# Performance work log

Hardware: AMD Instinct MI355X
Metric: run time of the kernel (lower is better)

## Reference

```python
import jax, jax.numpy as jnp
import numpy as np

B, C, D = 32768, 1000, 512
ALPHA, BETA = 1.0, 1.0
TEMPERATURE = 0.1


def setup_inputs() -> dict:
    key = jax.random.key(0)
    k1, k2, k3, k4 = jax.random.split(key, 4)
    return {
        "features_front": jax.random.normal(k1, (B, D), dtype=jnp.float32),
        "logits": jax.random.normal(k2, (B, C), dtype=jnp.float32),
        "labels": jax.random.randint(k3, (B,), 0, C, dtype=jnp.int64),
        "text_prototype": jax.random.normal(k4, (C, D), dtype=jnp.float32),
    }


def reference(features_front, logits, labels, text_prototype):
    num_class = text_prototype.shape[0]

    # F.cross_entropy (mean reduction)
    logp = jax.nn.log_softmax(logits, axis=-1)
    loss_ce = -jnp.mean(jnp.take_along_axis(logp, labels[:, None], axis=1)[:, 0])

    # F.normalize(prototypes, dim=1)
    norm = jnp.linalg.norm(text_prototype, axis=1, keepdims=True)
    prototypes = text_prototype / jnp.maximum(norm, 1e-12)

    # supervised contrastive term against class prototypes
    feat_dot_prototype = (features_front @ prototypes.T) / TEMPERATURE  # [B, C]
    logits_max = jax.lax.stop_gradient(jnp.max(feat_dot_prototype, axis=1, keepdims=True))
    lg = feat_dot_prototype - logits_max
    log_prob = lg - jnp.log(jnp.sum(jnp.exp(lg), axis=1, keepdims=True))
    mask = (labels[:, None] == jnp.arange(num_class)[None, :]).astype(log_prob.dtype)
    mean_log_prob_pos = jnp.sum(mask * log_prob, axis=1)
    simloss = -jnp.mean(mean_log_prob_pos)

    # prototype repulsion: sum_{i != j} exp(p_i . p_j) == masked exp-sum of Gram matrix
    gram = prototypes @ prototypes.T  # [C, C]
    offdiag = 1.0 - jnp.eye(num_class, dtype=gram.dtype)
    textloss = jnp.log(jnp.sum(jnp.exp(gram) * offdiag)) / num_class

    return ALPHA * simloss + BETA * loss_ce + textloss
```

## Files before the change

kernel.cpp:

```cpp
#include <hip/hip_runtime.h>
#include <math.h>

#define NB 32768
#define NC 1000
#define ND 512
#define LOG2E 1.4426950408889634f
#define LN2 0.6931471805599453f
#define S2 14.426950408889634f
#define OFF2 79.3482272f
#define OFFLN 55.0f
#define NBUCKET 64

typedef __attribute__((ext_vector_type(8))) short short8;
typedef __attribute__((ext_vector_type(16))) float f32x16;

__device__ __forceinline__ float fexp2(float x) {
    float r; asm("v_exp_f32 %0, %1" : "=v"(r) : "v"(x)); return r;
}
__device__ __forceinline__ float flog2(float x) {
    float r; asm("v_log_f32 %0, %1" : "=v"(r) : "v"(x)); return r;
}
__device__ __forceinline__ unsigned short bf16_rne(float f) {
    unsigned int u = __builtin_bit_cast(unsigned int, f);
    u += 0x7FFFu + ((u >> 16) & 1u);
    return (unsigned short)(u >> 16);
}
__device__ __forceinline__ short8 pack8f(float4 a, float4 b) {
    short8 s;
    s[0] = (short)bf16_rne(a.x); s[1] = (short)bf16_rne(a.y);
    s[2] = (short)bf16_rne(a.z); s[3] = (short)bf16_rne(a.w);
    s[4] = (short)bf16_rne(b.x); s[5] = (short)bf16_rne(b.y);
    s[6] = (short)bf16_rne(b.z); s[7] = (short)bf16_rne(b.w);
    return s;
}

__device__ __forceinline__ void stage16k(const short8* __restrict__ src, short8* dst, int t) {
#pragma unroll
    for (int s = 0; s < 4; ++s) {
        const int id = t + 256 * s;
        __builtin_amdgcn_global_load_lds(
            (const __attribute__((address_space(1))) unsigned int*)(src + id),
            (__attribute__((address_space(3))) unsigned int*)(dst + id), 16, 0, 0);
    }
}

__global__ __launch_bounds__(256) void norm_protos(const float* __restrict__ pro,
                                                   unsigned short* __restrict__ pbf) {
    const int row = blockIdx.x, t = threadIdx.x;
    const int grp = row >> 5, l31 = row & 31;
    const int ks = t >> 3, h = (t >> 2) & 1, p = t & 3;
    const int k0 = ks * 16 + 8 * h + 2 * p;
    unsigned int* dst = (unsigned int*)pbf +
        ((size_t)(grp * 32 + ks) * 64 + h * 32 + l31) * 4 + p;
    if (row >= NC) { *dst = 0u; return; }
    const float* rp = pro + (size_t)row * ND;
    const float x0 = rp[k0], x1 = rp[k0 + 1];
    float ss = x0 * x0 + x1 * x1;
#pragma unroll
    for (int o = 1; o < 64; o <<= 1) ss += __shfl_xor(ss, o, 64);
    __shared__ float part[4];
    if ((t & 63) == 0) part[t >> 6] = ss;
    __syncthreads();
    const float nrm = sqrtf(part[0] + part[1] + part[2] + part[3]);
    const float sc = 1.0f / fmaxf(nrm, 1e-12f);
    *dst = (unsigned int)bf16_rne(x0 * sc) | ((unsigned int)bf16_rne(x1 * sc) << 16);
}

__global__ __launch_bounds__(256, 2) void fat_kernel(const float* __restrict__ feat,
                                                     const float* __restrict__ logits,
                                                     const int* __restrict__ labels,
                                                     const unsigned short* __restrict__ pbf,
                                                     float* __restrict__ buckets,
                                                     float2* __restrict__ part) {
    __shared__ short8 lds0[1024], lds1[1024];
    __shared__ float wsum[4];
    const int r5 = blockIdx.x % 5;
    const int q = blockIdx.x / 5;
    const int t = threadIdx.x;
    const int wid = t >> 6, lane = t & 63;
    const short8* frag = (const short8*)pbf;

    if (r5 == 0 || r5 == 2) {
        const int idx = q * 2 + (r5 == 2);
        const int rb = idx >> 1, ch = idx & 1;
        const int gbase = ch * 16;
        const int l31 = lane & 31, h = lane >> 5;
        const int row = rb * 128 + wid * 32 + l31;

        stage16k(frag + gbase * 2048, lds0, t);

        short8 bf[32];
        {
            const float* fp = feat + (size_t)row * ND + 8 * h;
#pragma unroll
            for (int ks = 0; ks < 32; ++ks)
                bf[ks] = pack8f(*(const float4*)(fp + 16 * ks), *(const float4*)(fp + 16 * ks + 4));
        }
        int lab = labels[row];
        lab = lab < 0 ? 0 : (lab > NC - 1 ? NC - 1 : lab);
        const int labg = lab >> 5, labc = lab & 31;

        float ls = 0.f, lv = 0.f;
        __syncthreads();

#pragma unroll 1
        for (int g = 0; g < 16; ++g) {
            const int gg = gbase + g;
            stage16k(frag + gg * 2048 + 1024, lds1, t);
            f32x16 acc = {};
#pragma unroll
            for (int ks = 0; ks < 16; ++ks)
                acc = __builtin_amdgcn_mfma_f32_32x32x16_bf16(lds0[ks * 64 + lane], bf[ks], acc, 0, 0, 0);
            __syncthreads();
            if (g < 15) stage16k(frag + (gg + 1) * 2048, lds0, t);
#pragma unroll
            for (int ks = 0; ks < 16; ++ks)
                acc = __builtin_amdgcn_mfma_f32_32x32x16_bf16(lds1[ks * 64 + lane], bf[16 + ks], acc, 0, 0, 0);
#pragma unroll
            for (int r = 0; r < 16; ++r) ls += fexp2(fmaf(acc[r], S2, -OFF2));
            if (labg == gg) {
#pragma unroll
                for (int r = 0; r < 16; ++r) {
                    const int cls = (r & 3) + 8 * (r >> 2) + 4 * h;
                    lv += (cls == labc) ? acc[r] : 0.f;
                }
            }
            __syncthreads();
        }

        ls += __shfl_xor(ls, 32, 64);
        lv += __shfl_xor(lv, 32, 64);
        if (lane < 32) {
            float2 p; p.x = ls; p.y = lv;
            part[(size_t)row * 2 + ch] = p;
        }

    } else if (r5 != 4) {
        const int idx = q * 2 + (r5 == 3);
        const int rowbase = idx * 64 + wid * 16;
        const int q4 = lane >> 4, l16 = lane & 15;
        float localce = 0.f;
#pragma unroll 1
        for (int i = 0; i < 4; ++i) {
            const int row = rowbase + 4 * i + q4;
            const float* rp = logits + (size_t)row * NC;
            const float4* rp4 = (const float4*)rp;
            float s = 0.f;
#pragma unroll
            for (int j = 0; j < 15; ++j) {
                const float4 v = rp4[l16 + 16 * j];
                s += fexp2(v.x * LOG2E) + fexp2(v.y * LOG2E) +
                     fexp2(v.z * LOG2E) + fexp2(v.w * LOG2E);
            }
            if (l16 < 10) {
                const float4 v = rp4[l16 + 240];
                s += fexp2(v.x * LOG2E) + fexp2(v.y * LOG2E) +
                     fexp2(v.z * LOG2E) + fexp2(v.w * LOG2E);
            }
#pragma unroll
            for (int o = 1; o <= 8; o <<= 1) s += __shfl_xor(s, o, 64);
            if (l16 == 0) {
                int lab = labels[row];
                lab = lab < 0 ? 0 : (lab > NC - 1 ? NC - 1 : lab);
                localce += flog2(s) * LN2 - rp[lab];
            }
        }
#pragma unroll
        for (int o = 1; o < 64; o <<= 1) localce += __shfl_xor(localce, o, 64);
        if (lane == 0) wsum[wid] = localce;
        __syncthreads();
        if (t == 0)
            atomicAdd(buckets + 1024 + (idx & (NBUCKET - 1)) * 16,
                      (wsum[0] + wsum[1] + wsum[2] + wsum[3]) * (1.0f / (float)NB));

    } else {
        const int ct = q >> 3;
        const int bg = q & 7;
        const int btile = bg * 4 + wid;
        const int l31 = lane & 31, h = lane >> 5;

        f32x16 acc = {};
#pragma unroll
        for (int ks = 0; ks < 32; ++ks)
            acc = __builtin_amdgcn_mfma_f32_32x32x16_bf16(frag[(size_t)(ct * 32 + ks) * 64 + lane],
                                                          frag[(size_t)(btile * 32 + ks) * 64 + lane],
                                                          acc, 0, 0, 0);
        const int jg = btile * 32 + l31;
        float s = 0.f;
        if (jg < NC) {
#pragma unroll
            for (int r = 0; r < 16; ++r) {
                const int ig = ct * 32 + (r & 3) + 8 * (r >> 2) + 4 * h;
                if (ig < NC && ig != jg) s += fexp2(acc[r] * LOG2E);
            }
        }
#pragma unroll
        for (int o = 1; o < 64; o <<= 1) s += __shfl_xor(s, o, 64);
        if (lane == 0) wsum[wid] = s;
        __syncthreads();
        if (t == 0)
            atomicAdd(buckets + 2048 + (q & (NBUCKET - 1)) * 16,
                      wsum[0] + wsum[1] + wsum[2] + wsum[3]);
    }
}

__global__ __launch_bounds__(256) void simmerge_kernel(const float2* __restrict__ part,
                                                       float* __restrict__ buckets) {
    __shared__ float wsum[4];
    const int t = threadIdx.x, wid = t >> 6, lane = t & 63;
    const int row = blockIdx.x * 256 + t;
    const float2 p0 = part[(size_t)row * 2];
    const float2 p1 = part[(size_t)row * 2 + 1];
    float v = (OFFLN + flog2(p0.x + p1.x) * LN2 - 10.0f * (p0.y + p1.y)) * (1.0f / (float)NB);
#pragma unroll
    for (int o = 1; o < 64; o <<= 1) v += __shfl_xor(v, o, 64);
    if (lane == 0) wsum[wid] = v;
    __syncthreads();
    if (t == 0)
        atomicAdd(buckets + (blockIdx.x & (NBUCKET - 1)) * 16,
                  wsum[0] + wsum[1] + wsum[2] + wsum[3]);
}

__global__ void combine_kernel(const float* __restrict__ a, float* __restrict__ out) {
    const int t = threadIdx.x;
    float s = a[t * 16], c = a[1024 + t * 16], gr = a[2048 + t * 16];
#pragma unroll
    for (int o = 1; o < 64; o <<= 1) {
        s += __shfl_xor(s, o, 64);
        c += __shfl_xor(c, o, 64);
        gr += __shfl_xor(gr, o, 64);
    }
    if (t == 0) out[0] = s + c + logf(gr) * (1.0f / (float)NC);
}

extern "C" void kernel_launch(void* const* d_in, const int* in_sizes, int n_in,
                              void* d_out, int out_size, void* d_ws, size_t ws_size,
                              hipStream_t stream) {
    const float* feat   = (const float*)d_in[0];
    const float* logits = (const float*)d_in[1];
    const int*   labels = (const int*)d_in[2];
    const float* pro    = (const float*)d_in[3];
    float* out = (float*)d_out;

    float* acc = (float*)d_ws;
    unsigned short* pbf = (unsigned short*)((char*)d_ws + 16384);
    float2* part = (float2*)((char*)d_ws + (2u << 20));

    hipMemsetAsync(d_ws, 0, 3072 * sizeof(float), stream);
    hipLaunchKernelGGL(norm_protos,     dim3(1024), dim3(256), 0, stream, pro, pbf);
    hipLaunchKernelGGL(fat_kernel,      dim3(1280), dim3(256), 0, stream,
                       feat, logits, labels, pbf, acc, part);
    hipLaunchKernelGGL(simmerge_kernel, dim3(128),  dim3(256), 0, stream, part, acc);
    hipLaunchKernelGGL(combine_kernel,  dim3(1),    dim3(64),  0, stream, acc, out);
}
```

Baseline: 110.6 us.

## Switch fused kernel to 16x16x32 MFMA tiles with finer block decomposition

Changes the prototype bf16 fragment layout to 16-class tiles and rewrites the similarity GEMM to use 16x16x32 MFMA with two interleaved accumulators. Each block now handles 64 feature rows and half the classes, which cuts per-thread register fragments from 32 to 16 and trims padding from 1024 to 1008 classes. The grid grows to 3072 blocks with a 3-way role split, so logits CE and Gram blocks also get smaller work units. The aim is higher occupancy and balance, at the cost of more blocks, more LDS staging steps per class and more redundant feature loads per class tile.

```diff
diff --git a/kernel.cpp b/kernel.cpp
--- a/kernel.cpp
+++ b/kernel.cpp
@@ -12,7 +12,7 @@
 #define NBUCKET 64
 
 typedef __attribute__((ext_vector_type(8))) short short8;
-typedef __attribute__((ext_vector_type(16))) float f32x16;
+typedef __attribute__((ext_vector_type(4))) float f32x4;
 
 __device__ __forceinline__ float fexp2(float x) {
     float r; asm("v_exp_f32 %0, %1" : "=v"(r) : "v"(x)); return r;
@@ -47,14 +47,13 @@
 __global__ __launch_bounds__(256) void norm_protos(const float* __restrict__ pro,
                                                    unsigned short* __restrict__ pbf) {
     const int row = blockIdx.x, t = threadIdx.x;
-    const int grp = row >> 5, l31 = row & 31;
-    const int ks = t >> 3, h = (t >> 2) & 1, p = t & 3;
-    const int k0 = ks * 16 + 8 * h + 2 * p;
+    const int tile = row >> 4, r = row & 15;
+    const int kk = t >> 4, g = (t >> 2) & 3, slot = t & 3;
     unsigned int* dst = (unsigned int*)pbf +
-        ((size_t)(grp * 32 + ks) * 64 + h * 32 + l31) * 4 + p;
+        ((size_t)tile * 1024 + kk * 64 + g * 16 + r) * 4 + slot;
     if (row >= NC) { *dst = 0u; return; }
     const float* rp = pro + (size_t)row * ND;
-    const float x0 = rp[k0], x1 = rp[k0 + 1];
+    const float x0 = rp[2 * t], x1 = rp[2 * t + 1];
     float ss = x0 * x0 + x1 * x1;
 #pragma unroll
     for (int o = 1; o < 64; o <<= 1) ss += __shfl_xor(ss, o, 64);
@@ -74,74 +73,70 @@
                                                      float2* __restrict__ part) {
     __shared__ short8 lds0[1024], lds1[1024];
     __shared__ float wsum[4];
-    const int r5 = blockIdx.x % 5;
-    const int q = blockIdx.x / 5;
+    const int role = blockIdx.x % 3;
+    const int idx = blockIdx.x / 3;
     const int t = threadIdx.x;
     const int wid = t >> 6, lane = t & 63;
     const short8* frag = (const short8*)pbf;
 
-    if (r5 == 0 || r5 == 2) {
-        const int idx = q * 2 + (r5 == 2);
+    if (role == 0) {
         const int rb = idx >> 1, ch = idx & 1;
-        const int gbase = ch * 16;
-        const int l31 = lane & 31, h = lane >> 5;
-        const int row = rb * 128 + wid * 32 + l31;
-
-        stage16k(frag + gbase * 2048, lds0, t);
-
-        short8 bf[32];
+        const int t0 = ch ? 32 : 0;
+        const int nt = ch ? 31 : 32;
+        const int r16 = lane & 15, g = lane >> 4;
+        const int row = rb * 64 + wid * 16 + r16;
+
+        stage16k(frag + t0 * 1024, lds0, t);
+
+        short8 bf[16];
         {
-            const float* fp = feat + (size_t)row * ND + 8 * h;
-#pragma unroll
-            for (int ks = 0; ks < 32; ++ks)
-                bf[ks] = pack8f(*(const float4*)(fp + 16 * ks), *(const float4*)(fp + 16 * ks + 4));
+            const float* fp = feat + (size_t)row * ND + 8 * g;
+#pragma unroll
+            for (int kk = 0; kk < 16; ++kk)
+                bf[kk] = pack8f(*(const float4*)(fp + 32 * kk), *(const float4*)(fp + 32 * kk + 4));
         }
         int lab = labels[row];
         lab = lab < 0 ? 0 : (lab > NC - 1 ? NC - 1 : lab);
-        const int labg = lab >> 5, labc = lab & 31;
 
         float ls = 0.f, lv = 0.f;
         __syncthreads();
 
 #pragma unroll 1
-        for (int g = 0; g < 16; ++g) {
-            const int gg = gbase + g;
-            stage16k(frag + gg * 2048 + 1024, lds1, t);
-            f32x16 acc = {};
-#pragma unroll
-            for (int ks = 0; ks < 16; ++ks)
-                acc = __builtin_amdgcn_mfma_f32_32x32x16_bf16(lds0[ks * 64 + lane], bf[ks], acc, 0, 0, 0);
+        for (int j = 0; j < nt; ++j) {
+            const short8* cur = (j & 1) ? lds1 : lds0;
+            if (j + 1 < nt) stage16k(frag + (t0 + j + 1) * 1024, (j & 1) ? lds0 : lds1, t);
+
+            f32x4 aE = {0.f, 0.f, 0.f, 0.f}, aO = {0.f, 0.f, 0.f, 0.f};
+#pragma unroll
+            for (int kk = 0; kk < 8; ++kk) {
+                aE = __builtin_amdgcn_mfma_f32_16x16x32_bf16(cur[kk * 64 + lane], bf[kk], aE, 0, 0, 0);
+                aO = __builtin_amdgcn_mfma_f32_16x16x32_bf16(cur[(8 + kk) * 64 + lane], bf[8 + kk], aO, 0, 0, 0);
+            }
+            const int cbase = (t0 + j) * 16 + g * 4;
+#pragma unroll
+            for (int rI = 0; rI < 4; ++rI) {
+                const float d = aE[rI] + aO[rI];
+                ls += fexp2(fmaf(d, S2, -OFF2));
+                lv += (cbase + rI == lab) ? d : 0.f;
+            }
             __syncthreads();
-            if (g < 15) stage16k(frag + (gg + 1) * 2048, lds0, t);
-#pragma unroll
-            for (int ks = 0; ks < 16; ++ks)
-                acc = __builtin_amdgcn_mfma_f32_32x32x16_bf16(lds1[ks * 64 + lane], bf[16 + ks], acc, 0, 0, 0);
-#pragma unroll
-            for (int r = 0; r < 16; ++r) ls += fexp2(fmaf(acc[r], S2, -OFF2));
-            if (labg == gg) {
-#pragma unroll
-                for (int r = 0; r < 16; ++r) {
-                    const int cls = (r & 3) + 8 * (r >> 2) + 4 * h;
-                    lv += (cls == labc) ? acc[r] : 0.f;
-                }
-            }
-            __syncthreads();
-        }
-
+        }
+
+        ls += __shfl_xor(ls, 16, 64);
+        lv += __shfl_xor(lv, 16, 64);
         ls += __shfl_xor(ls, 32, 64);
         lv += __shfl_xor(lv, 32, 64);
-        if (lane < 32) {
+        if (lane < 16) {
             float2 p; p.x = ls; p.y = lv;
             part[(size_t)row * 2 + ch] = p;
         }
 
-    } else if (r5 != 4) {
-        const int idx = q * 2 + (r5 == 3);
-        const int rowbase = idx * 64 + wid * 16;
+    } else if (role == 1) {
+        const int rowbase = idx * 32 + wid * 8;
         const int q4 = lane >> 4, l16 = lane & 15;
         float localce = 0.f;
 #pragma unroll 1
-        for (int i = 0; i < 4; ++i) {
+        for (int i = 0; i < 2; ++i) {
             const int row = rowbase + 4 * i + q4;
             const float* rp = logits + (size_t)row * NC;
             const float4* rp4 = (const float4*)rp;
@@ -174,24 +169,34 @@
                       (wsum[0] + wsum[1] + wsum[2] + wsum[3]) * (1.0f / (float)NB));
 
     } else {
-        const int ct = q >> 3;
-        const int bg = q & 7;
-        const int btile = bg * 4 + wid;
-        const int l31 = lane & 31, h = lane >> 5;
-
-        f32x16 acc = {};
-#pragma unroll
-        for (int ks = 0; ks < 32; ++ks)
-            acc = __builtin_amdgcn_mfma_f32_32x32x16_bf16(frag[(size_t)(ct * 32 + ks) * 64 + lane],
-                                                          frag[(size_t)(btile * 32 + ks) * 64 + lane],
-                                                          acc, 0, 0, 0);
-        const int jg = btile * 32 + l31;
+        if (idx >= 1008) return;
+        const int ct = idx >> 4;
+        const int bx = idx & 15;
+        const int r16 = lane & 15, g = lane >> 4;
+        const int btile = bx * 4 + wid;
+        const int irow = btile * 16 + r16;
+
+        f32x4 dacc = {0.f, 0.f, 0.f, 0.f};
+#pragma unroll 1
+        for (int pass = 0; pass < 2; ++pass) {
+            const int kb = pass * 8;
+            short8 af[8], bfr[8];
+#pragma unroll
+            for (int kk = 0; kk < 8; ++kk) {
+                af[kk]  = frag[(size_t)ct * 1024 + (kb + kk) * 64 + lane];
+                bfr[kk] = frag[(size_t)btile * 1024 + (kb + kk) * 64 + lane];
+            }
+#pragma unroll
+            for (int kk = 0; kk < 8; ++kk)
+                dacc = __builtin_amdgcn_mfma_f32_16x16x32_bf16(af[kk], bfr[kk], dacc, 0, 0, 0);
+        }
         float s = 0.f;
-        if (jg < NC) {
-#pragma unroll
-            for (int r = 0; r < 16; ++r) {
-                const int ig = ct * 32 + (r & 3) + 8 * (r >> 2) + 4 * h;
-                if (ig < NC && ig != jg) s += fexp2(acc[r] * LOG2E);
+        if (irow < NC) {
+            const int cbase = ct * 16 + g * 4;
+#pragma unroll
+            for (int rI = 0; rI < 4; ++rI) {
+                const int j = cbase + rI;
+                if (j < NC && j != irow) s += fexp2(dacc[rI] * LOG2E);
             }
         }
 #pragma unroll
@@ -199,7 +204,7 @@
         if (lane == 0) wsum[wid] = s;
         __syncthreads();
         if (t == 0)
-            atomicAdd(buckets + 2048 + (q & (NBUCKET - 1)) * 16,
+            atomicAdd(buckets + 2048 + (idx & (NBUCKET - 1)) * 16,
                       wsum[0] + wsum[1] + wsum[2] + wsum[3]);
     }
 }
@@ -248,7 +253,7 @@
 
     hipMemsetAsync(d_ws, 0, 3072 * sizeof(float), stream);
     hipLaunchKernelGGL(norm_protos,     dim3(1024), dim3(256), 0, stream, pro, pbf);
-    hipLaunchKernelGGL(fat_kernel,      dim3(1280), dim3(256), 0, stream,
+    hipLaunchKernelGGL(fat_kernel,      dim3(3072), dim3(256), 0, stream,
                        feat, logits, labels, pbf, acc, part);
     hipLaunchKernelGGL(simmerge_kernel, dim3(128),  dim3(256), 0, stream, part, acc);
     hipLaunchKernelGGL(combine_kernel,  dim3(1),    dim3(64),  0, stream, acc, out);
```

New measurement: 100.1 us. 1.1x faster.
